# Kernel tuning notes

Hardware: AMD Instinct MI355X
Metric: run time of the kernel (lower is better)

Reference implementation:

```python
import jax, jax.numpy as jnp
import numpy as np
from jax import lax

B, S, F, D, H, L, A = 16, 512, 64, 512, 8, 4, 3
E = D // H  # head_dim = 64

def _gelu(t):
    return jax.nn.gelu(t, approximate=False)  # torch nn.GELU() is exact erf

def _make_masks():
    i = jnp.arange(S)[:, None]
    j = jnp.arange(S)[None, :]
    d = jnp.abs(i - j)
    ms = []
    for h in range(min(5, H)):
        dil = 2 ** h
        ms.append((d <= dil) | (d % (2 ** (h + 1)) == 0))
    m = jnp.stack(ms)  # [5,S,S] bool
    idx = jnp.minimum(jnp.arange(H), m.shape[0] - 1)
    return m[idx]  # [H,S,S]

MASKS = _make_masks()

def _ln(x, g, b, eps=1e-5):
    mu = jnp.mean(x, -1, keepdims=True)
    var = jnp.mean((x - mu) ** 2, -1, keepdims=True)
    return (x - mu) * lax.rsqrt(var + eps) * g + b

def _conv1d(x_ncw, w, b):
    y = lax.conv_general_dilated(x_ncw, w, (1,), [(1, 1)],
                                 dimension_numbers=("NCH", "OIH", "NCH"))
    return y + b[None, :, None]

def _attn(x, Wq, bq, Wk, bk, Wv, bv, Wo, bo):
    # x: [B,S,D]; Wq/Wk/Wv: [H,E,D] (stacked per-head Linear weights)
    q = jnp.einsum("bsd,hed->bhse", x, Wq) + bq[None, :, None, :]
    k = jnp.einsum("bsd,hed->bhse", x, Wk) + bk[None, :, None, :]
    v = jnp.einsum("bsd,hed->bhse", x, Wv) + bv[None, :, None, :]
    s = jnp.einsum("bhse,bhte->bhst", q, k) / (E ** 0.5)
    s = jnp.where(MASKS[None], s, -jnp.inf)  # log-sparse masked_fill
    p = jax.nn.softmax(s, axis=-1)
    o = jnp.einsum("bhst,bhte->bhse", p, v)
    o = o.transpose(0, 2, 1, 3).reshape(x.shape[0], x.shape[1], D)  # concat heads
    return o @ Wo.T + bo

def _forward(x, conv1_w, conv1_b, conv2_w, conv2_b, emb_w, emb_b, pos,
             Wq, bq, Wk, bk, Wv, bv, Wo, bo, ln1_g, ln1_b, ln2_g, ln2_b,
             W1, b1, W2, b2, lnf_g, lnf_b,
             a1_w, a1_b, a2_w, a2_b, a3_w, a3_b, a4_w, a4_b,
             c1_w, c1_b, c2_w, c2_b, c3_w, c3_b, c4_w, c4_b):
    # feature extractor: two conv1d+GELU over time axis
    h0 = _gelu(_conv1d(x.transpose(0, 2, 1), conv1_w, conv1_b))
    h0 = _gelu(_conv1d(h0, conv2_w, conv2_b)).transpose(0, 2, 1)  # [B,S,D]
    z = h0 @ emb_w.T + emb_b + pos[:, :S]  # input embedding + positional
    for l in range(L):  # PyraFormer blocks (pre-norm residual)
        z = z + _attn(_ln(z, ln1_g[l], ln1_b[l]),
                      Wq[l], bq[l], Wk[l], bk[l], Wv[l], bv[l], Wo[l], bo[l])
        h = _ln(z, ln2_g[l], ln2_b[l])
        z = z + (_gelu(h @ W1[l].T + b1[l]) @ W2[l].T + b2[l])
    z = _ln(z, lnf_g, lnf_b)
    feat = z[:, -1, :]  # last timestep features

    def head(f, layers):
        (w1, bb1), (w2, bb2), (w3, bb3), (w4, bb4) = layers
        f = _gelu(f @ w1.T + bb1)
        f = _gelu(f @ w2.T + bb2)
        f = _gelu(f @ w3.T + bb3)
        return f @ w4.T + bb4

    policy = head(feat, [(a1_w, a1_b), (a2_w, a2_b), (a3_w, a3_b), (a4_w, a4_b)])
    value = head(feat, [(c1_w, c1_b), (c2_w, c2_b), (c3_w, c3_b), (c4_w, c4_b)])
    return policy, value

def setup_inputs() -> dict:
    key = jax.random.key(0)
    ks = iter(jax.random.split(key, 64))
    r = lambda shape, s=0.05: jax.random.normal(next(ks), shape, jnp.float32) * s
    return {
        "x": jax.random.normal(next(ks), (B, S, F), jnp.float32),
        "conv1_w": r((D // 2, F, 3)), "conv1_b": jnp.zeros((D // 2,)),
        "conv2_w": r((D, D // 2, 3)), "conv2_b": jnp.zeros((D,)),
        "emb_w": r((D, D)), "emb_b": jnp.zeros((D,)),
        "pos": r((1, S, D), 0.02),
        "Wq": r((L, H, E, D)), "bq": jnp.zeros((L, H, E)),
        "Wk": r((L, H, E, D)), "bk": jnp.zeros((L, H, E)),
        "Wv": r((L, H, E, D)), "bv": jnp.zeros((L, H, E)),
        "Wo": r((L, D, D)), "bo": jnp.zeros((L, D)),
        "ln1_g": jnp.ones((L, D)), "ln1_b": jnp.zeros((L, D)),
        "ln2_g": jnp.ones((L, D)), "ln2_b": jnp.zeros((L, D)),
        "W1": r((L, 4 * D, D)), "b1": jnp.zeros((L, 4 * D)),
        "W2": r((L, D, 4 * D)), "b2": jnp.zeros((L, D)),
        "lnf_g": jnp.ones((D,)), "lnf_b": jnp.zeros((D,)),
        "a1_w": r((128, D)), "a1_b": jnp.zeros((128,)),
        "a2_w": r((256, 128)), "a2_b": jnp.zeros((256,)),
        "a3_w": r((57, 256)), "a3_b": jnp.zeros((57,)),
        "a4_w": r((A, 57)), "a4_b": jnp.zeros((A,)),
        "c1_w": r((128, D)), "c1_b": jnp.zeros((128,)),
        "c2_w": r((256, 128)), "c2_b": jnp.zeros((256,)),
        "c3_w": r((57, 256)), "c3_b": jnp.zeros((57,)),
        "c4_w": r((1, 57)), "c4_b": jnp.zeros((1,)),
    }

def reference(x, conv1_w, conv1_b, conv2_w, conv2_b, emb_w, emb_b, pos,
              Wq, bq, Wk, bk, Wv, bv, Wo, bo, ln1_g, ln1_b, ln2_g, ln2_b,
              W1, b1, W2, b2, lnf_g, lnf_b,
              a1_w, a1_b, a2_w, a2_b, a3_w, a3_b, a4_w, a4_b,
              c1_w, c1_b, c2_w, c2_b, c3_w, c3_b, c4_w, c4_b):
    return _forward(x, conv1_w, conv1_b, conv2_w, conv2_b, emb_w, emb_b, pos,
                    Wq, bq, Wk, bk, Wv, bv, Wo, bo, ln1_g, ln1_b, ln2_g, ln2_b,
                    W1, b1, W2, b2, lnf_g, lnf_b,
                    a1_w, a1_b, a2_w, a2_b, a3_w, a3_b, a4_w, a4_b,
                    c1_w, c1_b, c2_w, c2_b, c3_w, c3_b, c4_w, c4_b)
```

## Files before the change

kernel.cpp:

```cpp
#include <hip/hip_runtime.h>
#include <hip/hip_bf16.h>
#include <cstdint>

typedef __attribute__((ext_vector_type(8))) short bf16x8;
typedef __attribute__((ext_vector_type(4))) float f32x4;
typedef unsigned short u16;

#define DEV __device__ __forceinline__

DEV float b2f(u16 u) {
  union { unsigned int i; float f; } v; v.i = ((unsigned int)u) << 16; return v.f;
}
DEV u16 f2b(float f) {
  __hip_bfloat16 h = __float2bfloat16(f);
  return *reinterpret_cast<u16*>(&h);
}
DEV float erf_fast(float x) {
  float ax = fabsf(x);
  float t = __builtin_amdgcn_rcpf(fmaf(0.3275911f, ax, 1.0f));
  float p = t * fmaf(t, fmaf(t, fmaf(t, fmaf(t, 1.061405429f, -1.453152027f),
                                     1.421413741f), -0.284496736f), 0.254829592f);
  float r = fmaf(-p, __expf(-ax * ax), 1.0f);
  return copysignf(r, x);
}
DEV float gelu_f(float x) { return 0.5f * x * (1.0f + erf_fast(x * 0.70710678118654752f)); }

DEV void async_cp16(const u16* g, u16* l) {
  __builtin_amdgcn_global_load_lds(
      (const __attribute__((address_space(1))) void*)g,
      (__attribute__((address_space(3))) void*)l, 16, 0, 0);
}

__global__ void probe_kernel(const unsigned int* __restrict__ g, int* __restrict__ flag) {
  if (threadIdx.x == 0 && blockIdx.x == 0) *flag = (*g == 0x3F800000u) ? 1 : 0;
}

struct CvtArgs {
  const void* src[42];
  unsigned int off[43];
};

struct alignas(16) U8v { u16 u[8]; };
struct alignas(8)  U4v { u16 u[4]; };

__global__ __launch_bounds__(256) void cvt_kernel(CvtArgs a, int n_t, unsigned int total,
                                                  const int* __restrict__ flag,
                                                  u16* __restrict__ dst) {
  unsigned int i8 = (blockIdx.x * 256u + threadIdx.x) * 8u;
  if (i8 >= total) return;
  int t = 0;
  while (t + 1 < n_t && i8 >= a.off[t + 1]) t++;
  unsigned int j = i8 - a.off[t];
  bool in_seg = (i8 + 8 <= a.off[t + 1]) && (i8 + 8 <= total);
  int fp32 = *flag;
  if (fp32) {
    if (in_seg && ((j & 3) == 0)) {
      const float* s = (const float*)a.src[t] + j;
      float4 v0 = *(const float4*)s;
      float4 v1 = *(const float4*)(s + 4);
      U8v o;
      o.u[0] = f2b(v0.x); o.u[1] = f2b(v0.y); o.u[2] = f2b(v0.z); o.u[3] = f2b(v0.w);
      o.u[4] = f2b(v1.x); o.u[5] = f2b(v1.y); o.u[6] = f2b(v1.z); o.u[7] = f2b(v1.w);
      *(U8v*)(dst + i8) = o;
    } else {
      for (int k = 0; k < 8; k++) {
        unsigned int i = i8 + k;
        if (i >= total) break;
        int tt = t;
        while (tt + 1 < n_t && i >= a.off[tt + 1]) tt++;
        dst[i] = f2b(((const float*)a.src[tt])[i - a.off[tt]]);
      }
    }
  } else {
    if (in_seg && ((j & 7) == 0)) {
      *(U8v*)(dst + i8) = *(const U8v*)((const u16*)a.src[t] + j);
    } else {
      for (int k = 0; k < 8; k++) {
        unsigned int i = i8 + k;
        if (i >= total) break;
        int tt = t;
        while (tt + 1 < n_t && i >= a.off[tt + 1]) tt++;
        dst[i] = ((const u16*)a.src[tt])[i - a.off[tt]];
      }
    }
  }
}

__global__ __launch_bounds__(256) void xform_kernel(
    const u16* __restrict__ Wq, const u16* __restrict__ Wk, const u16* __restrict__ Wv,
    const u16* __restrict__ W1,
    const u16* __restrict__ bq, const u16* __restrict__ bk, const u16* __restrict__ bv,
    const u16* __restrict__ b1,
    const u16* __restrict__ ln1_g, const u16* __restrict__ ln1_b,
    const u16* __restrict__ ln2_g, const u16* __restrict__ ln2_b,
    float* __restrict__ stats, float* __restrict__ cvec)
{
  int bid = blockIdx.x;
  if (bid < 144) {
    int i = (bid * 256 + threadIdx.x) * 4;
    *(float4*)&stats[i] = (float4){0.f, 0.f, 0.f, 0.f};
    return;
  }
  int rid = (bid - 144) * 4 + (threadIdx.x >> 6);
  int l = rid / 3584;
  int rr = rid - l * 3584;
  const u16 *Wrow, *g, *b;
  float bias;
  float *c1p, *c2p;
  float* cl = cvec + l * 7168;
  if (rr < 1536) {
    int sel = rr >> 9, row = rr & 511;
    const u16* Wm = sel == 0 ? Wq : (sel == 1 ? Wk : Wv);
    const u16* bm = sel == 0 ? bq : (sel == 1 ? bk : bv);
    Wrow = Wm + (size_t)l * 262144 + (size_t)row * 512;
    g = ln1_g + l * 512; b = ln1_b + l * 512;
    bias = b2f(bm[l * 512 + row]);
    c1p = cl + sel * 1024 + row;
    c2p = cl + sel * 1024 + 512 + row;
  } else {
    int row = rr - 1536;
    Wrow = W1 + (size_t)l * 1048576 + (size_t)row * 512;
    g = ln2_g + l * 512; b = ln2_b + l * 512;
    bias = b2f(b1[l * 2048 + row]);
    c1p = cl + 3072 + row;
    c2p = cl + 3072 + 2048 + row;
  }
  int lane = threadIdx.x & 63;
  U8v wv = *(const U8v*)(Wrow + lane * 8);
  U8v gv = *(const U8v*)(g + lane * 8);
  U8v bv2 = *(const U8v*)(b + lane * 8);
  float s1 = 0.f, s2 = 0.f;
#pragma unroll
  for (int j = 0; j < 8; j++) {
    float w = b2f(wv.u[j]);
    s1 += w * b2f(gv.u[j]);
    s2 += w * b2f(bv2.u[j]);
  }
#pragma unroll
  for (int mm = 1; mm < 64; mm <<= 1) {
    s1 += __shfl_xor(s1, mm, 64);
    s2 += __shfl_xor(s2, mm, 64);
  }
  if (lane == 0) { *c1p = s1; *c2p = s2 + bias; }
}

__global__ __launch_bounds__(256) void gemm_bt44(
    const u16* __restrict__ A, const u16* __restrict__ W,
    const u16* __restrict__ bias,
    u16* __restrict__ outB, float* __restrict__ outF,
    const u16* __restrict__ pos,
    const u16* __restrict__ g_vec, float* __restrict__ stats, u16* __restrict__ zb,
    int N, int K, int mode)
{
  __shared__ __align__(16) u16 As[2][64 * 32];
  __shared__ __align__(16) u16 Bs[2][64 * 32];
  int t = threadIdx.x, l = t & 63, w = t >> 6;
  int wr = w >> 1, wc = w & 1;
  int col = l & 15, quad = l >> 4;
  int q8 = (quad ^ ((col >> 1) & 3)) * 8;
  int m0 = blockIdx.x * 64;
  int n0 = blockIdx.y * 64;

  f32x4 acc[2][2];
#pragma unroll
  for (int i = 0; i < 2; i++)
#pragma unroll
    for (int j = 0; j < 2; j++) acc[i][j] = (f32x4){0.f, 0.f, 0.f, 0.f};

  int ra = t >> 2;
  int ca = (t & 3) ^ ((ra >> 1) & 3);
  const u16* a1 = A + (size_t)(m0 + ra) * K + ca * 8;
  const u16* b1 = W + (size_t)(n0 + ra) * K + ca * 8;

  int nK = K >> 5;
  async_cp16(a1, &As[0][t * 8]);
  async_cp16(b1, &Bs[0][t * 8]);
  for (int ki = 0; ki < nK; ki++) {
    int cur = ki & 1;
    if (ki + 1 < nK) {
      int nxt = cur ^ 1, kt = (ki + 1) << 5;
      async_cp16(a1 + kt, &As[nxt][t * 8]);
      async_cp16(b1 + kt, &Bs[nxt][t * 8]);
      __builtin_amdgcn_s_waitcnt(0x0F72);
    } else {
      __builtin_amdgcn_s_waitcnt(0x0F70);
    }
    __builtin_amdgcn_s_barrier();
    __builtin_amdgcn_sched_barrier(0);
    bf16x8 af[2], bfv[2];
#pragma unroll
    for (int mi = 0; mi < 2; mi++)
      af[mi] = *(const bf16x8*)&As[cur][(wr * 32 + mi * 16 + col) * 32 + q8];
#pragma unroll
    for (int ni = 0; ni < 2; ni++)
      bfv[ni] = *(const bf16x8*)&Bs[cur][(wc * 32 + ni * 16 + col) * 32 + q8];
#pragma unroll
    for (int mi = 0; mi < 2; mi++)
#pragma unroll
      for (int ni = 0; ni < 2; ni++)
        acc[mi][ni] = __builtin_amdgcn_mfma_f32_16x16x32_bf16(bfv[ni], af[mi], acc[mi][ni], 0, 0, 0);
    __builtin_amdgcn_sched_barrier(0);
    __builtin_amdgcn_s_barrier();
  }

  int mBase = m0 + wr * 32, nBase = n0 + wc * 32;
  if (mode == 1) {
#pragma unroll
    for (int mi = 0; mi < 2; mi++) {
      int m = mBase + mi * 16 + col;
      size_t rowOff = (size_t)m * N;
#pragma unroll
      for (int ni = 0; ni < 2; ni++) {
        int n4 = nBase + ni * 16 + quad * 4;
        U4v bb = *(const U4v*)&bias[n4];
        f32x4 v = acc[mi][ni];
        U4v o;
#pragma unroll
        for (int r = 0; r < 4; r++) o.u[r] = f2b(gelu_f(v[r] + b2f(bb.u[r])));
        *(U4v*)&outB[rowOff + n4] = o;
      }
    }
  } else {
#pragma unroll
    for (int mi = 0; mi < 2; mi++) {
      int m = mBase + mi * 16 + col;
      size_t rowOff = (size_t)m * N;
      float s = 0.f, s2 = 0.f;
#pragma unroll
      for (int ni = 0; ni < 2; ni++) {
        int n4 = nBase + ni * 16 + quad * 4;
        U4v bb = *(const U4v*)&bias[n4];
        f32x4 v = acc[mi][ni];
        float4 zv;
        if (mode == 2) {
          float4 old = *(float4*)&outF[rowOff + n4];
          zv.x = old.x + v[0] + b2f(bb.u[0]);
          zv.y = old.y + v[1] + b2f(bb.u[1]);
          zv.z = old.z + v[2] + b2f(bb.u[2]);
          zv.w = old.w + v[3] + b2f(bb.u[3]);
        } else {
          U4v pp = *(const U4v*)&pos[(m & 511) * 512 + n4];
          zv.x = v[0] + b2f(bb.u[0]) + b2f(pp.u[0]);
          zv.y = v[1] + b2f(bb.u[1]) + b2f(pp.u[1]);
          zv.z = v[2] + b2f(bb.u[2]) + b2f(pp.u[2]);
          zv.w = v[3] + b2f(bb.u[3]) + b2f(pp.u[3]);
        }
        *(float4*)&outF[rowOff + n4] = zv;
        U4v gg = *(const U4v*)&g_vec[n4];
        U4v ob;
        ob.u[0] = f2b(zv.x * b2f(gg.u[0]));
        ob.u[1] = f2b(zv.y * b2f(gg.u[1]));
        ob.u[2] = f2b(zv.z * b2f(gg.u[2]));
        ob.u[3] = f2b(zv.w * b2f(gg.u[3]));
        *(U4v*)&zb[rowOff + n4] = ob;
        s  += zv.x + zv.y + zv.z + zv.w;
        s2 += zv.x * zv.x + zv.y * zv.y + zv.z * zv.z + zv.w * zv.w;
      }
      s  += __shfl_xor(s, 16, 64);  s  += __shfl_xor(s, 32, 64);
      s2 += __shfl_xor(s2, 16, 64); s2 += __shfl_xor(s2, 32, 64);
      if (quad == 0) {
        atomicAdd(&stats[2 * m], s);
        atomicAdd(&stats[2 * m + 1], s2);
      }
    }
  }
}

__global__ __launch_bounds__(256) void gemm_bt128x64(
    const u16* __restrict__ A, const u16* __restrict__ W,
    const float* __restrict__ stats,
    const float* __restrict__ c1, const float* __restrict__ c2,
    u16* __restrict__ outB, int N, int K)
{
  __shared__ __align__(16) u16 As[2][128 * 32];
  __shared__ __align__(16) u16 Bs[2][64 * 32];
  int t = threadIdx.x, l = t & 63, w = t >> 6;
  int wr = w >> 1, wc = w & 1;
  int col = l & 15, quad = l >> 4;
  int q8 = (quad ^ ((col >> 1) & 3)) * 8;
  int m0 = blockIdx.x * 128;
  int n0 = blockIdx.y * 64;

  f32x4 acc[4][2];
#pragma unroll
  for (int i = 0; i < 4; i++)
#pragma unroll
    for (int j = 0; j < 2; j++) acc[i][j] = (f32x4){0.f, 0.f, 0.f, 0.f};

  int g1i = t, g2i = t + 256;
  int r1 = g1i >> 2, r2 = g2i >> 2;
  int cb1 = (g1i & 3) ^ ((r1 >> 1) & 3);
  int cb2 = (g2i & 3) ^ ((r2 >> 1) & 3);
  int rb = t >> 2;
  int cbb = (t & 3) ^ ((rb >> 1) & 3);
  const u16* a1 = A + (size_t)(m0 + r1) * K + cb1 * 8;
  const u16* a2 = A + (size_t)(m0 + r2) * K + cb2 * 8;
  const u16* b1 = W + (size_t)(n0 + rb) * K + cbb * 8;

  int nK = K >> 5;
  async_cp16(a1, &As[0][g1i * 8]);
  async_cp16(a2, &As[0][g2i * 8]);
  async_cp16(b1, &Bs[0][t * 8]);
  for (int ki = 0; ki < nK; ki++) {
    int cur = ki & 1;
    if (ki + 1 < nK) {
      int nxt = cur ^ 1, kt = (ki + 1) << 5;
      async_cp16(a1 + kt, &As[nxt][g1i * 8]);
      async_cp16(a2 + kt, &As[nxt][g2i * 8]);
      async_cp16(b1 + kt, &Bs[nxt][t * 8]);
      __builtin_amdgcn_s_waitcnt(0x0F73);
    } else {
      __builtin_amdgcn_s_waitcnt(0x0F70);
    }
    __builtin_amdgcn_s_barrier();
    __builtin_amdgcn_sched_barrier(0);
    bf16x8 af[4], bfv[2];
#pragma unroll
    for (int mi = 0; mi < 4; mi++)
      af[mi] = *(const bf16x8*)&As[cur][(wr * 64 + mi * 16 + col) * 32 + q8];
#pragma unroll
    for (int ni = 0; ni < 2; ni++)
      bfv[ni] = *(const bf16x8*)&Bs[cur][(wc * 32 + ni * 16 + col) * 32 + q8];
#pragma unroll
    for (int mi = 0; mi < 4; mi++)
#pragma unroll
      for (int ni = 0; ni < 2; ni++)
        acc[mi][ni] = __builtin_amdgcn_mfma_f32_16x16x32_bf16(bfv[ni], af[mi], acc[mi][ni], 0, 0, 0);
    __builtin_amdgcn_sched_barrier(0);
    __builtin_amdgcn_s_barrier();
  }

  int mBase = m0 + wr * 64, nBase = n0 + wc * 32;
#pragma unroll
  for (int mi = 0; mi < 4; mi++) {
    int m = mBase + mi * 16 + col;
    size_t rowOff = (size_t)m * N;
    float st0 = stats[2 * m], st1 = stats[2 * m + 1];
    float mu = st0 * (1.0f / 512.0f);
    float var = st1 * (1.0f / 512.0f) - mu * mu;
    float rs = rsqrtf(var + 1e-5f);
    float nmu = rs * mu;
#pragma unroll
    for (int ni = 0; ni < 2; ni++) {
      int n4 = nBase + ni * 16 + quad * 4;
      float4 c1v = *(const float4*)&c1[n4];
      float4 c2v = *(const float4*)&c2[n4];
      f32x4 v = acc[mi][ni];
      U4v o;
      o.u[0] = f2b(gelu_f(rs * v[0] - nmu * c1v.x + c2v.x));
      o.u[1] = f2b(gelu_f(rs * v[1] - nmu * c1v.y + c2v.y));
      o.u[2] = f2b(gelu_f(rs * v[2] - nmu * c1v.z + c2v.z));
      o.u[3] = f2b(gelu_f(rs * v[3] - nmu * c1v.w + c2v.w));
      *(U4v*)&outB[rowOff + n4] = o;
    }
  }
}

__global__ __launch_bounds__(256) void gemm_qkv256(
    const u16* __restrict__ A,
    const u16* __restrict__ Wq, const u16* __restrict__ Wk, const u16* __restrict__ Wv,
    const float* __restrict__ stats, const float* __restrict__ cv,
    u16* __restrict__ outQ, u16* __restrict__ outK, u16* __restrict__ outVT, int K)
{
  __shared__ __align__(16) u16 As[2][64 * 32];
  __shared__ __align__(16) u16 Bs[2][256 * 32];
  int t = threadIdx.x, l = t & 63, w = t >> 6;
  int wr = w >> 1, wc = w & 1;
  int col = l & 15, quad = l >> 4;
  int q8 = (quad ^ ((col >> 1) & 3)) * 8;
  int m0 = blockIdx.x * 64;
  int sel = blockIdx.y >> 1;
  int n0 = (blockIdx.y & 1) * 256;
  const u16* W = sel == 0 ? Wq : (sel == 1 ? Wk : Wv);
  const float* c1 = cv + sel * 1024;
  const float* c2 = c1 + 512;
  const bool swp = (sel < 2);
  const float scl = sel == 0 ? 0.125f : 1.0f;

  f32x4 acc[2][8];
#pragma unroll
  for (int i = 0; i < 2; i++)
#pragma unroll
    for (int j = 0; j < 8; j++) acc[i][j] = (f32x4){0.f, 0.f, 0.f, 0.f};

  int ra = t >> 2;
  int ca = (t & 3) ^ ((ra >> 1) & 3);
  const u16* a1 = A + (size_t)(m0 + ra) * K + ca * 8;
  const u16* bptr[4];
  int bidx[4];
#pragma unroll
  for (int j = 0; j < 4; j++) {
    int gi = t + 256 * j;
    int rb = gi >> 2;
    int cb = (gi & 3) ^ ((rb >> 1) & 3);
    bptr[j] = W + (size_t)(n0 + rb) * K + cb * 8;
    bidx[j] = gi;
  }

  int nK = K >> 5;
  async_cp16(a1, &As[0][t * 8]);
#pragma unroll
  for (int j = 0; j < 4; j++) async_cp16(bptr[j], &Bs[0][bidx[j] * 8]);
  for (int ki = 0; ki < nK; ki++) {
    int cur = ki & 1;
    if (ki + 1 < nK) {
      int nxt = cur ^ 1, kt = (ki + 1) << 5;
      async_cp16(a1 + kt, &As[nxt][t * 8]);
#pragma unroll
      for (int j = 0; j < 4; j++) async_cp16(bptr[j] + kt, &Bs[nxt][bidx[j] * 8]);
      __builtin_amdgcn_s_waitcnt(0x0F75);
    } else {
      __builtin_amdgcn_s_waitcnt(0x0F70);
    }
    __builtin_amdgcn_s_barrier();
    __builtin_amdgcn_sched_barrier(0);
    bf16x8 af[2], bfv[8];
#pragma unroll
    for (int mi = 0; mi < 2; mi++)
      af[mi] = *(const bf16x8*)&As[cur][(wr * 32 + mi * 16 + col) * 32 + q8];
#pragma unroll
    for (int ni = 0; ni < 8; ni++)
      bfv[ni] = *(const bf16x8*)&Bs[cur][(wc * 128 + ni * 16 + col) * 32 + q8];
    if (swp) {
#pragma unroll
      for (int mi = 0; mi < 2; mi++)
#pragma unroll
        for (int ni = 0; ni < 8; ni++)
          acc[mi][ni] = __builtin_amdgcn_mfma_f32_16x16x32_bf16(bfv[ni], af[mi], acc[mi][ni], 0, 0, 0);
    } else {
#pragma unroll
      for (int mi = 0; mi < 2; mi++)
#pragma unroll
        for (int ni = 0; ni < 8; ni++)
          acc[mi][ni] = __builtin_amdgcn_mfma_f32_16x16x32_bf16(af[mi], bfv[ni], acc[mi][ni], 0, 0, 0);
    }
    __builtin_amdgcn_sched_barrier(0);
    __builtin_amdgcn_s_barrier();
  }

  int mBase = m0 + wr * 32, nBase = n0 + wc * 128;
  if (swp) {
    u16* outB = sel == 0 ? outQ : outK;
#pragma unroll
    for (int mi = 0; mi < 2; mi++) {
      int m = mBase + mi * 16 + col;
      size_t rowOff = (size_t)m * 512;
      float st0 = stats[2 * m], st1 = stats[2 * m + 1];
      float mu = st0 * (1.0f / 512.0f);
      float var = st1 * (1.0f / 512.0f) - mu * mu;
      float rs = rsqrtf(var + 1e-5f);
      float nmu = rs * mu;
#pragma unroll
      for (int ni = 0; ni < 8; ni++) {
        int n4 = nBase + ni * 16 + quad * 4;
        float4 c1v = *(const float4*)&c1[n4];
        float4 c2v = *(const float4*)&c2[n4];
        f32x4 v = acc[mi][ni];
        U4v o;
        o.u[0] = f2b((rs * v[0] - nmu * c1v.x + c2v.x) * scl);
        o.u[1] = f2b((rs * v[1] - nmu * c1v.y + c2v.y) * scl);
        o.u[2] = f2b((rs * v[2] - nmu * c1v.z + c2v.z) * scl);
        o.u[3] = f2b((rs * v[3] - nmu * c1v.w + c2v.w) * scl);
        *(U4v*)&outB[rowOff + n4] = o;
      }
    }
  } else {
    int b = m0 >> 9;
    int sB = m0 & 511;
#pragma unroll
    for (int mi = 0; mi < 2; mi++) {
      int mb4 = m0 + wr * 32 + mi * 16 + quad * 4;
      int s4 = sB + wr * 32 + mi * 16 + quad * 4;
      float rs_r[4], nmu_r[4];
#pragma unroll
      for (int r = 0; r < 4; r++) {
        float st0 = stats[2 * (mb4 + r)], st1 = stats[2 * (mb4 + r) + 1];
        float mu = st0 * (1.0f / 512.0f);
        float var = st1 * (1.0f / 512.0f) - mu * mu;
        float rs = rsqrtf(var + 1e-5f);
        rs_r[r] = rs; nmu_r[r] = rs * mu;
      }
#pragma unroll
      for (int ni = 0; ni < 8; ni++) {
        int n = nBase + ni * 16 + col;
        int h = n >> 6, e = n & 63;
        float c1s = c1[n], c2s = c2[n];
        f32x4 v = acc[mi][ni];
        U4v o;
#pragma unroll
        for (int r = 0; r < 4; r++)
          o.u[r] = f2b(rs_r[r] * v[r] - nmu_r[r] * c1s + c2s);
        *(U4v*)&outVT[((size_t)((b * 8 + h) * 64 + e)) * 512 + s4] = o;
      }
    }
  }
}

__global__ void im2col3_kernel(const u16* __restrict__ src,
                               u16* __restrict__ dst, int C)
{
  int m = blockIdx.x;
  int k = blockIdx.y * blockDim.x + threadIdx.x;
  int ci = k / 3;
  int tap = k - ci * 3;
  int s = m & 511;
  int sp = s + tap - 1;
  u16 val = 0;
  if (sp >= 0 && sp < 512) val = src[(size_t)(m + tap - 1) * C + ci];
  dst[(size_t)m * (3 * C) + k] = val;
}

__global__ __launch_bounds__(256) void lnf_kernel(
    const float* __restrict__ z, const u16* __restrict__ gam,
    const u16* __restrict__ bet, u16* __restrict__ feat)
{
  int w = threadIdx.x >> 6, l = threadIdx.x & 63;
  int b = blockIdx.x * 4 + w;
  const float* zr = z + ((size_t)b * 512 + 511) * 512;
  float4 v0 = *(const float4*)(zr + l * 8);
  float4 v1 = *(const float4*)(zr + l * 8 + 4);
  float x[8] = {v0.x, v0.y, v0.z, v0.w, v1.x, v1.y, v1.z, v1.w};
  float s = 0.f;
#pragma unroll
  for (int i = 0; i < 8; i++) s += x[i];
#pragma unroll
  for (int mm = 1; mm < 64; mm <<= 1) s += __shfl_xor(s, mm, 64);
  float mu = s * (1.0f / 512.0f);
  float vs = 0.f;
#pragma unroll
  for (int i = 0; i < 8; i++) { float d = x[i] - mu; vs += d * d; }
#pragma unroll
  for (int mm = 1; mm < 64; mm <<= 1) vs += __shfl_xor(vs, mm, 64);
  float rs = rsqrtf(vs * (1.0f / 512.0f) + 1e-5f);
  U8v gg = *(const U8v*)(gam + l * 8);
  U8v bb = *(const U8v*)(bet + l * 8);
  U8v o;
#pragma unroll
  for (int i = 0; i < 8; i++) o.u[i] = f2b((x[i] - mu) * rs * b2f(gg.u[i]) + b2f(bb.u[i]));
  *(U8v*)(feat + (size_t)b * 512 + l * 8) = o;
}

#define AST 72
__global__ __launch_bounds__(256) void attn_kernel(
    const u16* __restrict__ Q, const u16* __restrict__ Kg,
    const u16* __restrict__ VT, u16* __restrict__ O)
{
  __shared__ __align__(16) u16 Ks[64 * AST];
  __shared__ __align__(16) u16 Vts[64 * AST];
  __shared__ __align__(16) u16 Ps[64 * AST];
  const float NEG = -1e30f;
  int blk = blockIdx.x;
  int bh = blk & 127;
  int i0 = (blk >> 7) * 64;
  int b = bh >> 3, h = bh & 7;
  int t = threadIdx.x, w = t >> 6, l = t & 63;
  int col = l & 15, quad = l >> 4;
  int dil = 1 << (h < 4 ? h : 4);
  int per_m1 = 2 * dil - 1;

  {
    int row = t >> 2, c = (t & 3) * 16;
    const u16* src = Q + ((size_t)(b * 512 + i0 + row) * 512 + h * 64 + c);
    *(float4*)&Ps[row * AST + c] = *(const float4*)src;
    *(float4*)&Ps[row * AST + c + 8] = *(const float4*)(src + 8);
  }
  __builtin_amdgcn_s_waitcnt(0xC07F);
  __builtin_amdgcn_sched_barrier(0);
  bf16x8 qa[2];
#pragma unroll
  for (int kk = 0; kk < 2; kk++)
    qa[kk] = *(const bf16x8*)&Ps[(w * 16 + col) * AST + kk * 32 + quad * 8];

  f32x4 acc_o[4];
#pragma unroll
  for (int i = 0; i < 4; i++) acc_o[i] = (f32x4){0.f, 0.f, 0.f, 0.f};
  float m_run = NEG, l_run = 0.f;
  int ig = i0 + w * 16 + col;

  for (int jt = 0; jt < 8; jt++) {
    int j0 = jt * 64;
    {
      int row = t >> 2, c = (t & 3) * 16;
      const u16* ks = Kg + ((size_t)(b * 512 + j0 + row) * 512 + h * 64 + c);
      *(float4*)&Ks[row * AST + c] = *(const float4*)ks;
      *(float4*)&Ks[row * AST + c + 8] = *(const float4*)(ks + 8);
      const u16* vs = VT + ((size_t)(bh * 64 + row) * 512 + j0 + c);
      *(float4*)&Vts[row * AST + c] = *(const float4*)vs;
      *(float4*)&Vts[row * AST + c + 8] = *(const float4*)(vs + 8);
    }
    __syncthreads();

    f32x4 sa[4];
    __builtin_amdgcn_s_setprio(1);
#pragma unroll
    for (int ni = 0; ni < 4; ni++) {
      f32x4 s = (f32x4){0.f, 0.f, 0.f, 0.f};
#pragma unroll
      for (int kk = 0; kk < 2; kk++) {
        bf16x8 kb = *(const bf16x8*)&Ks[(ni * 16 + col) * AST + kk * 32 + quad * 8];
        s = __builtin_amdgcn_mfma_f32_16x16x32_bf16(kb, qa[kk], s, 0, 0, 0);
      }
      sa[ni] = s;
    }
    __builtin_amdgcn_s_setprio(0);

    float mx = NEG;
#pragma unroll
    for (int ni = 0; ni < 4; ni++)
#pragma unroll
      for (int r = 0; r < 4; r++) {
        int jg = j0 + ni * 16 + quad * 4 + r;
        int d = ig - jg; d = d < 0 ? -d : d;
        bool keep = (d <= dil) || ((d & per_m1) == 0);
        float s = keep ? sa[ni][r] : NEG;
        sa[ni][r] = s;
        mx = fmaxf(mx, s);
      }
    mx = fmaxf(mx, __shfl_xor(mx, 16, 64));
    mx = fmaxf(mx, __shfl_xor(mx, 32, 64));
    float mN = fmaxf(m_run, mx);
    float alpha = __expf(m_run - mN);
    m_run = mN;
    float rsum = 0.f;
#pragma unroll
    for (int ni = 0; ni < 4; ni++)
#pragma unroll
      for (int r = 0; r < 4; r++) {
        float p = __expf(sa[ni][r] - mN);
        sa[ni][r] = p;
        rsum += p;
      }
    rsum += __shfl_xor(rsum, 16, 64);
    rsum += __shfl_xor(rsum, 32, 64);
    l_run = l_run * alpha + rsum;

#pragma unroll
    for (int ni = 0; ni < 4; ni++) {
      unsigned int lo = (unsigned int)f2b(sa[ni][0]) | ((unsigned int)f2b(sa[ni][1]) << 16);
      unsigned int hi = (unsigned int)f2b(sa[ni][2]) | ((unsigned int)f2b(sa[ni][3]) << 16);
      uint2 pk; pk.x = lo; pk.y = hi;
      *(uint2*)&Ps[(w * 16 + col) * AST + ni * 16 + quad * 4] = pk;
    }
    __builtin_amdgcn_s_waitcnt(0xC07F);
    __builtin_amdgcn_sched_barrier(0);

    float a_sh[4];
#pragma unroll
    for (int r = 0; r < 4; r++) a_sh[r] = __shfl(alpha, quad * 4 + r, 64);
#pragma unroll
    for (int ne = 0; ne < 4; ne++)
#pragma unroll
      for (int r = 0; r < 4; r++) acc_o[ne][r] *= a_sh[r];

    bf16x8 pa[2];
#pragma unroll
    for (int kk = 0; kk < 2; kk++)
      pa[kk] = *(const bf16x8*)&Ps[(w * 16 + col) * AST + kk * 32 + quad * 8];
    __builtin_amdgcn_s_setprio(1);
#pragma unroll
    for (int ne = 0; ne < 4; ne++) {
#pragma unroll
      for (int kk = 0; kk < 2; kk++) {
        bf16x8 vb = *(const bf16x8*)&Vts[(ne * 16 + col) * AST + kk * 32 + quad * 8];
        acc_o[ne] = __builtin_amdgcn_mfma_f32_16x16x32_bf16(pa[kk], vb, acc_o[ne], 0, 0, 0);
      }
    }
    __builtin_amdgcn_s_setprio(0);
    __syncthreads();
  }

  float inv[4];
#pragma unroll
  for (int r = 0; r < 4; r++) {
    float lr = __shfl(l_run, quad * 4 + r, 64);
    inv[r] = 1.0f / fmaxf(lr, 1e-20f);
  }
#pragma unroll
  for (int ne = 0; ne < 4; ne++)
#pragma unroll
    for (int r = 0; r < 4; r++) {
      float o = acc_o[ne][r] * inv[r];
      O[((size_t)(b * 512 + i0 + w * 16 + quad * 4 + r)) * 512 + h * 64 + ne * 16 + col] = f2b(o);
    }
}

__global__ __launch_bounds__(256) void heads_kernel(
    const u16* __restrict__ feat,
    const u16* __restrict__ a1w, const u16* __restrict__ a1b,
    const u16* __restrict__ a2w, const u16* __restrict__ a2b,
    const u16* __restrict__ a3w, const u16* __restrict__ a3b,
    const u16* __restrict__ a4w, const u16* __restrict__ a4b,
    const u16* __restrict__ c1w, const u16* __restrict__ c1b,
    const u16* __restrict__ c2w, const u16* __restrict__ c2b,
    const u16* __restrict__ c3w, const u16* __restrict__ c3b,
    const u16* __restrict__ c4w, const u16* __restrict__ c4b,
    const int* __restrict__ flag, void* __restrict__ outv)
{
  __shared__ float f[512];
  __shared__ float g1[256];
  __shared__ float g2[512];
  __shared__ float g3[128];
  int b = blockIdx.x, t = threadIdx.x;
  f[t] = b2f(feat[b * 512 + t]);
  f[t + 256] = b2f(feat[b * 512 + 256 + t]);
  __syncthreads();
  {
    const u16* wrow; float bias;
    if (t < 128) { wrow = a1w + (size_t)t * 512; bias = b2f(a1b[t]); }
    else { wrow = c1w + (size_t)(t - 128) * 512; bias = b2f(c1b[t - 128]); }
    float s = bias;
    for (int k = 0; k < 512; k += 8) {
      U8v wv = *(const U8v*)(wrow + k);
#pragma unroll
      for (int j = 0; j < 8; j++) s += b2f(wv.u[j]) * f[k + j];
    }
    g1[t] = gelu_f(s);
  }
  __syncthreads();
  {
    float s1 = b2f(a2b[t]);
    for (int k = 0; k < 128; k += 8) {
      U8v wv = *(const U8v*)(a2w + (size_t)t * 128 + k);
#pragma unroll
      for (int j = 0; j < 8; j++) s1 += b2f(wv.u[j]) * g1[k + j];
    }
    float s2 = b2f(c2b[t]);
    for (int k = 0; k < 128; k += 8) {
      U8v wv = *(const U8v*)(c2w + (size_t)t * 128 + k);
#pragma unroll
      for (int j = 0; j < 8; j++) s2 += b2f(wv.u[j]) * g1[128 + k + j];
    }
    g2[t] = gelu_f(s1);
    g2[256 + t] = gelu_f(s2);
  }
  __syncthreads();
  if (t < 57) {
    float s = b2f(a3b[t]);
    for (int k = 0; k < 256; k += 8) {
      U8v wv = *(const U8v*)(a3w + (size_t)t * 256 + k);
#pragma unroll
      for (int j = 0; j < 8; j++) s += b2f(wv.u[j]) * g2[k + j];
    }
    g3[t] = gelu_f(s);
  } else if (t >= 64 && t < 121) {
    int u = t - 64;
    float s = b2f(c3b[u]);
    for (int k = 0; k < 256; k += 8) {
      U8v wv = *(const U8v*)(c3w + (size_t)u * 256 + k);
#pragma unroll
      for (int j = 0; j < 8; j++) s += b2f(wv.u[j]) * g2[256 + k + j];
    }
    g3[64 + u] = gelu_f(s);
  }
  __syncthreads();
  int fp32out = *flag;
  if (t < 3) {
    float s = b2f(a4b[t]);
    for (int k = 0; k < 57; k++) s += b2f(a4w[t * 57 + k]) * g3[k];
    if (fp32out) ((float*)outv)[b * 3 + t] = s;
    else ((u16*)outv)[b * 3 + t] = f2b(s);
  } else if (t == 4) {
    float s = b2f(c4b[0]);
    for (int k = 0; k < 57; k++) s += b2f(c4w[k]) * g3[64 + k];
    if (fp32out) ((float*)outv)[48 + b] = s;
    else ((u16*)outv)[48 + b] = f2b(s);
  }
}

extern "C" void kernel_launch(void* const* d_in, const int* in_sizes, int n_in,
                              void* d_out, int out_size, void* d_ws, size_t ws_size,
                              hipStream_t stream)
{
  char* ws = (char*)d_ws;
  float* z    = (float*)ws;
  u16* R      = (u16*)(ws + (16u << 20));
  u16* bufQ   = R;
  u16* bufK   = (u16*)(ws + (24u << 20));
  u16* bufO   = (u16*)(ws + (32u << 20));
  u16* bufC   = (u16*)(ws + (32u << 20));
  u16* bufVT  = (u16*)(ws + (40u << 20));
  u16* zb     = (u16*)(ws + (48u << 20));
  u16* bufH   = (u16*)(ws + (48u << 20));
  u16* feat   = R;
  u16* pool   = (u16*)(ws + (56u << 20));
  float* stats = (float*)(ws + (84u << 20));
  float* cvec  = (float*)(ws + (85u << 20));
  int* flag   = (int*)(ws + (88u << 20));

  CvtArgs args;
  unsigned int off = 0;
  int nt = n_in < 42 ? n_in : 42;
  for (int i = 0; i < nt; i++) { args.src[i] = d_in[i]; args.off[i] = off; off += (unsigned int)in_sizes[i]; }
  args.off[nt] = off;
  unsigned int total = off;

  probe_kernel<<<1, 64, 0, stream>>>((const unsigned int*)d_in[24], flag);
  cvt_kernel<<<(total + 2047) / 2048, 256, 0, stream>>>(args, nt, total, flag, pool);

  const u16* P[42];
  for (int i = 0; i < nt; i++) P[i] = pool + args.off[i];
  const u16* x       = P[0];
  const u16* conv1_w = P[1];  const u16* conv1_b = P[2];
  const u16* conv2_w = P[3];  const u16* conv2_b = P[4];
  const u16* emb_w   = P[5];  const u16* emb_b   = P[6];
  const u16* pos     = P[7];
  const u16* Wq      = P[8];  const u16* bq      = P[9];
  const u16* Wk      = P[10]; const u16* bk      = P[11];
  const u16* Wv      = P[12]; const u16* bv      = P[13];
  const u16* Wo      = P[14]; const u16* bo      = P[15];
  const u16* ln1_g   = P[16]; const u16* ln1_b   = P[17];
  const u16* ln2_g   = P[18]; const u16* ln2_b   = P[19];
  const u16* W1      = P[20]; const u16* b1      = P[21];
  const u16* W2      = P[22]; const u16* b2      = P[23];
  const u16* lnf_g   = P[24]; const u16* lnf_b   = P[25];

  xform_kernel<<<3728, 256, 0, stream>>>(Wq, Wk, Wv, W1, bq, bk, bv, b1,
      ln1_g, ln1_b, ln2_g, ln2_b, stats, cvec);

  im2col3_kernel<<<dim3(8192, 1), 192, 0, stream>>>(x, R, 64);
  gemm_bt44<<<dim3(128, 4), 256, 0, stream>>>(R, conv1_w, conv1_b, bufH, nullptr,
      nullptr, nullptr, nullptr, nullptr, 256, 192, 1);
  im2col3_kernel<<<dim3(8192, 3), 256, 0, stream>>>(bufH, R, 256);
  gemm_bt44<<<dim3(128, 8), 256, 0, stream>>>(R, conv2_w, conv2_b, bufC, nullptr,
      nullptr, nullptr, nullptr, nullptr, 512, 768, 1);
  gemm_bt44<<<dim3(128, 8), 256, 0, stream>>>(bufC, emb_w, emb_b, nullptr, z,
      pos, ln1_g, stats, zb, 512, 512, 4);

  for (int l = 0; l < 4; l++) {
    float* cl = cvec + l * 7168;
    gemm_qkv256<<<dim3(128, 6), 256, 0, stream>>>(zb,
        Wq + (size_t)l * 262144, Wk + (size_t)l * 262144, Wv + (size_t)l * 262144,
        stats + (size_t)(2 * l) * 16384, cl, bufQ, bufK, bufVT, 512);
    attn_kernel<<<dim3(1024), 256, 0, stream>>>(bufQ, bufK, bufVT, bufO);
    gemm_bt44<<<dim3(128, 8), 256, 0, stream>>>(bufO, Wo + (size_t)l * 262144,
        bo + l * 512, nullptr, z, nullptr, ln2_g + l * 512,
        stats + (size_t)(2 * l + 1) * 16384, zb, 512, 512, 2);
    gemm_bt128x64<<<dim3(64, 32), 256, 0, stream>>>(zb, W1 + (size_t)l * 1048576,
        stats + (size_t)(2 * l + 1) * 16384, cl + 3072, cl + 3072 + 2048, R, 2048, 512);
    gemm_bt44<<<dim3(128, 8), 256, 0, stream>>>(R, W2 + (size_t)l * 1048576,
        b2 + l * 512, nullptr, z, nullptr, ln1_g + (l < 3 ? (l + 1) : 3) * 512,
        stats + (size_t)(2 * l + 2) * 16384, zb, 512, 2048, 2);
  }

  lnf_kernel<<<4, 256, 0, stream>>>(z, lnf_g, lnf_b, feat);
  heads_kernel<<<16, 256, 0, stream>>>(feat,
      P[26], P[27], P[28], P[29], P[30], P[31], P[32], P[33],
      P[34], P[35], P[36], P[37], P[38], P[39], P[40], P[41],
      flag, d_out);
}
```

Measured before the change: 924.8 us.

## Fuse Q projection into attention kernel and shrink KV GEMM tile

The Q projection (with the folded LayerNorm and the 1/sqrt(E) scale) moves out of the QKV GEMM and into the attention kernel. Each attention block now computes its own 64x64 Q tile from zb and Wq, using the K/V shared buffers as double-buffered staging, then writes the result into the Ps tile. The remaining K/V GEMM uses 128-wide N tiles over a 128x8 grid. This removes the Q round trip through global memory, at the cost of extra per-block GEMM work and one more __syncthreads before attention starts.

```diff
diff --git a/kernel.cpp b/kernel.cpp
--- a/kernel.cpp
+++ b/kernel.cpp
@@ -356,91 +356,85 @@
   }
 }
 
-__global__ __launch_bounds__(256) void gemm_qkv256(
+__global__ __launch_bounds__(256) void gemm_kv128(
     const u16* __restrict__ A,
-    const u16* __restrict__ Wq, const u16* __restrict__ Wk, const u16* __restrict__ Wv,
+    const u16* __restrict__ Wk, const u16* __restrict__ Wv,
     const float* __restrict__ stats, const float* __restrict__ cv,
-    u16* __restrict__ outQ, u16* __restrict__ outK, u16* __restrict__ outVT, int K)
+    u16* __restrict__ outK, u16* __restrict__ outVT, int K)
 {
   __shared__ __align__(16) u16 As[2][64 * 32];
-  __shared__ __align__(16) u16 Bs[2][256 * 32];
+  __shared__ __align__(16) u16 Bs[2][128 * 32];
   int t = threadIdx.x, l = t & 63, w = t >> 6;
   int wr = w >> 1, wc = w & 1;
   int col = l & 15, quad = l >> 4;
   int q8 = (quad ^ ((col >> 1) & 3)) * 8;
   int m0 = blockIdx.x * 64;
-  int sel = blockIdx.y >> 1;
-  int n0 = (blockIdx.y & 1) * 256;
-  const u16* W = sel == 0 ? Wq : (sel == 1 ? Wk : Wv);
-  const float* c1 = cv + sel * 1024;
+  int sel2 = blockIdx.y >> 2;
+  int n0 = (blockIdx.y & 3) * 128;
+  const u16* W = sel2 == 0 ? Wk : Wv;
+  const float* c1 = cv + (sel2 == 0 ? 1024 : 2048);
   const float* c2 = c1 + 512;
-  const bool swp = (sel < 2);
-  const float scl = sel == 0 ? 0.125f : 1.0f;
-
-  f32x4 acc[2][8];
+  const bool swp = (sel2 == 0);
+
+  f32x4 acc[2][4];
 #pragma unroll
   for (int i = 0; i < 2; i++)
 #pragma unroll
-    for (int j = 0; j < 8; j++) acc[i][j] = (f32x4){0.f, 0.f, 0.f, 0.f};
+    for (int j = 0; j < 4; j++) acc[i][j] = (f32x4){0.f, 0.f, 0.f, 0.f};
 
   int ra = t >> 2;
   int ca = (t & 3) ^ ((ra >> 1) & 3);
+  int g1i = t, g2i = t + 256;
+  int rb1 = g1i >> 2, rb2 = g2i >> 2;
+  int cb1 = (g1i & 3) ^ ((rb1 >> 1) & 3);
+  int cb2 = (g2i & 3) ^ ((rb2 >> 1) & 3);
   const u16* a1 = A + (size_t)(m0 + ra) * K + ca * 8;
-  const u16* bptr[4];
-  int bidx[4];
-#pragma unroll
-  for (int j = 0; j < 4; j++) {
-    int gi = t + 256 * j;
-    int rb = gi >> 2;
-    int cb = (gi & 3) ^ ((rb >> 1) & 3);
-    bptr[j] = W + (size_t)(n0 + rb) * K + cb * 8;
-    bidx[j] = gi;
-  }
+  const u16* b1 = W + (size_t)(n0 + rb1) * K + cb1 * 8;
+  const u16* b2 = W + (size_t)(n0 + rb2) * K + cb2 * 8;
 
   int nK = K >> 5;
   async_cp16(a1, &As[0][t * 8]);
-#pragma unroll
-  for (int j = 0; j < 4; j++) async_cp16(bptr[j], &Bs[0][bidx[j] * 8]);
+  async_cp16(b1, &Bs[0][g1i * 8]);
+  async_cp16(b2, &Bs[0][g2i * 8]);
   for (int ki = 0; ki < nK; ki++) {
     int cur = ki & 1;
     if (ki + 1 < nK) {
       int nxt = cur ^ 1, kt = (ki + 1) << 5;
       async_cp16(a1 + kt, &As[nxt][t * 8]);
-#pragma unroll
-      for (int j = 0; j < 4; j++) async_cp16(bptr[j] + kt, &Bs[nxt][bidx[j] * 8]);
-      __builtin_amdgcn_s_waitcnt(0x0F75);
+      async_cp16(b1 + kt, &Bs[nxt][g1i * 8]);
+      async_cp16(b2 + kt, &Bs[nxt][g2i * 8]);
+      __builtin_amdgcn_s_waitcnt(0x0F73);
     } else {
       __builtin_amdgcn_s_waitcnt(0x0F70);
     }
     __builtin_amdgcn_s_barrier();
     __builtin_amdgcn_sched_barrier(0);
-    bf16x8 af[2], bfv[8];
+    bf16x8 af[2], bfv[4];
 #pragma unroll
     for (int mi = 0; mi < 2; mi++)
       af[mi] = *(const bf16x8*)&As[cur][(wr * 32 + mi * 16 + col) * 32 + q8];
 #pragma unroll
-    for (int ni = 0; ni < 8; ni++)
-      bfv[ni] = *(const bf16x8*)&Bs[cur][(wc * 128 + ni * 16 + col) * 32 + q8];
+    for (int ni = 0; ni < 4; ni++)
+      bfv[ni] = *(const bf16x8*)&Bs[cur][(wc * 64 + ni * 16 + col) * 32 + q8];
     if (swp) {
 #pragma unroll
       for (int mi = 0; mi < 2; mi++)
 #pragma unroll
-        for (int ni = 0; ni < 8; ni++)
+        for (int ni = 0; ni < 4; ni++)
           acc[mi][ni] = __builtin_amdgcn_mfma_f32_16x16x32_bf16(bfv[ni], af[mi], acc[mi][ni], 0, 0, 0);
     } else {
 #pragma unroll
       for (int mi = 0; mi < 2; mi++)
 #pragma unroll
-        for (int ni = 0; ni < 8; ni++)
+        for (int ni = 0; ni < 4; ni++)
           acc[mi][ni] = __builtin_amdgcn_mfma_f32_16x16x32_bf16(af[mi], bfv[ni], acc[mi][ni], 0, 0, 0);
     }
     __builtin_amdgcn_sched_barrier(0);
     __builtin_amdgcn_s_barrier();
   }
 
-  int mBase = m0 + wr * 32, nBase = n0 + wc * 128;
+  int mBase = m0 + wr * 32, nBase = n0 + wc * 64;
   if (swp) {
-    u16* outB = sel == 0 ? outQ : outK;
 #pragma unroll
     for (int mi = 0; mi < 2; mi++) {
       int m = mBase + mi * 16 + col;
@@ -451,17 +445,17 @@
       float rs = rsqrtf(var + 1e-5f);
       float nmu = rs * mu;
 #pragma unroll
-      for (int ni = 0; ni < 8; ni++) {
+      for (int ni = 0; ni < 4; ni++) {
         int n4 = nBase + ni * 16 + quad * 4;
         float4 c1v = *(const float4*)&c1[n4];
         float4 c2v = *(const float4*)&c2[n4];
         f32x4 v = acc[mi][ni];
         U4v o;
-        o.u[0] = f2b((rs * v[0] - nmu * c1v.x + c2v.x) * scl);
-        o.u[1] = f2b((rs * v[1] - nmu * c1v.y + c2v.y) * scl);
-        o.u[2] = f2b((rs * v[2] - nmu * c1v.z + c2v.z) * scl);
-        o.u[3] = f2b((rs * v[3] - nmu * c1v.w + c2v.w) * scl);
-        *(U4v*)&outB[rowOff + n4] = o;
+        o.u[0] = f2b(rs * v[0] - nmu * c1v.x + c2v.x);
+        o.u[1] = f2b(rs * v[1] - nmu * c1v.y + c2v.y);
+        o.u[2] = f2b(rs * v[2] - nmu * c1v.z + c2v.z);
+        o.u[3] = f2b(rs * v[3] - nmu * c1v.w + c2v.w);
+        *(U4v*)&outK[rowOff + n4] = o;
       }
     }
   } else {
@@ -481,7 +475,7 @@
         rs_r[r] = rs; nmu_r[r] = rs * mu;
       }
 #pragma unroll
-      for (int ni = 0; ni < 8; ni++) {
+      for (int ni = 0; ni < 4; ni++) {
         int n = nBase + ni * 16 + col;
         int h = n >> 6, e = n & 63;
         float c1s = c1[n], c2s = c2[n];
@@ -542,8 +536,10 @@
 
 #define AST 72
 __global__ __launch_bounds__(256) void attn_kernel(
-    const u16* __restrict__ Q, const u16* __restrict__ Kg,
-    const u16* __restrict__ VT, u16* __restrict__ O)
+    const u16* __restrict__ zb, const u16* __restrict__ Wq,
+    const u16* __restrict__ Kg, const u16* __restrict__ VT,
+    const float* __restrict__ stats, const float* __restrict__ cv,
+    u16* __restrict__ O)
 {
   __shared__ __align__(16) u16 Ks[64 * AST];
   __shared__ __align__(16) u16 Vts[64 * AST];
@@ -555,17 +551,78 @@
   int b = bh >> 3, h = bh & 7;
   int t = threadIdx.x, w = t >> 6, l = t & 63;
   int col = l & 15, quad = l >> 4;
+  int wr = w >> 1, wc = w & 1;
+  int q8 = (quad ^ ((col >> 1) & 3)) * 8;
   int dil = 1 << (h < 4 ? h : 4);
   int per_m1 = 2 * dil - 1;
 
   {
-    int row = t >> 2, c = (t & 3) * 16;
-    const u16* src = Q + ((size_t)(b * 512 + i0 + row) * 512 + h * 64 + c);
-    *(float4*)&Ps[row * AST + c] = *(const float4*)src;
-    *(float4*)&Ps[row * AST + c + 8] = *(const float4*)(src + 8);
-  }
-  __builtin_amdgcn_s_waitcnt(0xC07F);
-  __builtin_amdgcn_sched_barrier(0);
+    f32x4 qacc[2][2];
+#pragma unroll
+    for (int i = 0; i < 2; i++)
+#pragma unroll
+      for (int j = 0; j < 2; j++) qacc[i][j] = (f32x4){0.f, 0.f, 0.f, 0.f};
+    int ra = t >> 2;
+    int ca = (t & 3) ^ ((ra >> 1) & 3);
+    const u16* a1 = zb + (size_t)(b * 512 + i0 + ra) * 512 + ca * 8;
+    const u16* b1 = Wq + (size_t)(h * 64 + ra) * 512 + ca * 8;
+    u16* AsQ = Ks;
+    u16* BsQ = Vts;
+    async_cp16(a1, &AsQ[t * 8]);
+    async_cp16(b1, &BsQ[t * 8]);
+    for (int ki = 0; ki < 16; ki++) {
+      int cur = ki & 1;
+      if (ki + 1 < 16) {
+        int nxt = cur ^ 1, kt = (ki + 1) << 5;
+        async_cp16(a1 + kt, &AsQ[nxt * 2048 + t * 8]);
+        async_cp16(b1 + kt, &BsQ[nxt * 2048 + t * 8]);
+        __builtin_amdgcn_s_waitcnt(0x0F72);
+      } else {
+        __builtin_amdgcn_s_waitcnt(0x0F70);
+      }
+      __builtin_amdgcn_s_barrier();
+      __builtin_amdgcn_sched_barrier(0);
+      bf16x8 af[2], bfv[2];
+#pragma unroll
+      for (int mi = 0; mi < 2; mi++)
+        af[mi] = *(const bf16x8*)&AsQ[cur * 2048 + (wr * 32 + mi * 16 + col) * 32 + q8];
+#pragma unroll
+      for (int ni = 0; ni < 2; ni++)
+        bfv[ni] = *(const bf16x8*)&BsQ[cur * 2048 + (wc * 32 + ni * 16 + col) * 32 + q8];
+#pragma unroll
+      for (int mi = 0; mi < 2; mi++)
+#pragma unroll
+        for (int ni = 0; ni < 2; ni++)
+          qacc[mi][ni] = __builtin_amdgcn_mfma_f32_16x16x32_bf16(bfv[ni], af[mi], qacc[mi][ni], 0, 0, 0);
+      __builtin_amdgcn_sched_barrier(0);
+      __builtin_amdgcn_s_barrier();
+    }
+#pragma unroll
+    for (int mi = 0; mi < 2; mi++) {
+      int m = wr * 32 + mi * 16 + col;
+      int g = b * 512 + i0 + m;
+      float st0 = stats[2 * g], st1 = stats[2 * g + 1];
+      float mu = st0 * (1.0f / 512.0f);
+      float var = st1 * (1.0f / 512.0f) - mu * mu;
+      float rs = rsqrtf(var + 1e-5f);
+      float nmu = rs * mu;
+#pragma unroll
+      for (int ni = 0; ni < 2; ni++) {
+        int n4l = wc * 32 + ni * 16 + quad * 4;
+        float4 c1v = *(const float4*)&cv[h * 64 + n4l];
+        float4 c2v = *(const float4*)&cv[512 + h * 64 + n4l];
+        f32x4 v = qacc[mi][ni];
+        U4v o;
+        o.u[0] = f2b((rs * v[0] - nmu * c1v.x + c2v.x) * 0.125f);
+        o.u[1] = f2b((rs * v[1] - nmu * c1v.y + c2v.y) * 0.125f);
+        o.u[2] = f2b((rs * v[2] - nmu * c1v.z + c2v.z) * 0.125f);
+        o.u[3] = f2b((rs * v[3] - nmu * c1v.w + c2v.w) * 0.125f);
+        *(U4v*)&Ps[m * AST + n4l] = o;
+      }
+    }
+  }
+  __syncthreads();
+
   bf16x8 qa[2];
 #pragma unroll
   for (int kk = 0; kk < 2; kk++)
@@ -774,7 +831,6 @@
   char* ws = (char*)d_ws;
   float* z    = (float*)ws;
   u16* R      = (u16*)(ws + (16u << 20));
-  u16* bufQ   = R;
   u16* bufK   = (u16*)(ws + (24u << 20));
   u16* bufO   = (u16*)(ws + (32u << 20));
   u16* bufC   = (u16*)(ws + (32u << 20));
@@ -828,10 +884,12 @@
 
   for (int l = 0; l < 4; l++) {
     float* cl = cvec + l * 7168;
-    gemm_qkv256<<<dim3(128, 6), 256, 0, stream>>>(zb,
-        Wq + (size_t)l * 262144, Wk + (size_t)l * 262144, Wv + (size_t)l * 262144,
-        stats + (size_t)(2 * l) * 16384, cl, bufQ, bufK, bufVT, 512);
-    attn_kernel<<<dim3(1024), 256, 0, stream>>>(bufQ, bufK, bufVT, bufO);
+    float* stl = stats + (size_t)(2 * l) * 16384;
+    gemm_kv128<<<dim3(128, 8), 256, 0, stream>>>(zb,
+        Wk + (size_t)l * 262144, Wv + (size_t)l * 262144,
+        stl, cl, bufK, bufVT, 512);
+    attn_kernel<<<dim3(1024), 256, 0, stream>>>(zb, Wq + (size_t)l * 262144,
+        bufK, bufVT, stl, cl, bufO);
     gemm_bt44<<<dim3(128, 8), 256, 0, stream>>>(bufO, Wo + (size_t)l * 262144,
         bo + l * 512, nullptr, z, nullptr, ln2_g + l * 512,
         stats + (size_t)(2 * l + 1) * 16384, zb, 512, 512, 2);
```

Result: faster. 885.7 us (-4.2%).
